# Kernel tuning notes

Hardware: AMD Instinct MI355X
Metric: run time of the kernel (lower is better)

The kernel has to match this reference:

```python
import jax, jax.numpy as jnp
import numpy as np

COUNT_CLIP_MAX = 1000.0

def _mlp2(x, w1, b1, w2, b2):
    # sg2im-style build_mlp with final_nonlinearity=True: relu after every linear
    h = jax.nn.relu(x @ w1 + b1)
    return jax.nn.relu(h @ w2 + b2)

def setup_inputs() -> dict:
    key = jax.random.key(0)
    ks = jax.random.split(key, 12)
    O, T, D, H = 100000, 400000, 128, 128
    D_out = D
    obj_vecs = jax.random.normal(ks[0], (O, D), dtype=jnp.float32)
    predi_vecs = jax.random.normal(ks[1], (T, D), dtype=jnp.float32)
    edges = jax.random.randint(ks[2], (T, 2), 0, O, dtype=jnp.int32)
    s = 0.02
    # net1: [3D, H, 2H + D_out]
    w1a = jax.random.normal(ks[3], (3 * D, H), dtype=jnp.float32) * s
    b1a = jnp.zeros((H,), dtype=jnp.float32)
    w1b = jax.random.normal(ks[4], (H, 2 * H + D_out), dtype=jnp.float32) * s
    b1b = jnp.zeros((2 * H + D_out,), dtype=jnp.float32)
    # net2: [H, H, D_out]
    w2a = jax.random.normal(ks[5], (H, H), dtype=jnp.float32) * s
    b2a = jnp.zeros((H,), dtype=jnp.float32)
    w2b = jax.random.normal(ks[6], (H, D_out), dtype=jnp.float32) * s
    b2b = jnp.zeros((D_out,), dtype=jnp.float32)
    return dict(obj_vecs=obj_vecs, predi_vecs=predi_vecs, edges=edges,
                w1a=w1a, b1a=b1a, w1b=w1b, b1b=b1b,
                w2a=w2a, b2a=b2a, w2b=w2b, b2b=b2b)

def reference(obj_vecs, predi_vecs, edges, w1a, b1a, w1b, b1b, w2a, b2a, w2b, b2b):
    O = obj_vecs.shape[0]
    H = w1a.shape[1]
    D_out = w2b.shape[1]
    s_idx = edges[:, 0]
    o_idx = edges[:, 1]
    # gather subject/object vectors, concat with predicate vecs: (T, 3D)
    cur_t_vecs = jnp.concatenate([obj_vecs[s_idx], predi_vecs, obj_vecs[o_idx]], axis=1)
    new_t_vecs = _mlp2(cur_t_vecs, w1a, b1a, w1b, b1b)  # (T, 2H + D_out)
    new_s_vecs = new_t_vecs[:, :H]
    new_p_vecs = new_t_vecs[:, H:H + D_out]
    new_o_vecs = new_t_vecs[:, H + D_out:2 * H + D_out]
    # scatter-add back to objects
    pooled = jnp.zeros((O, H), dtype=obj_vecs.dtype)
    pooled = pooled.at[s_idx].add(new_s_vecs).at[o_idx].add(new_o_vecs)
    # avg pooling: divide by clipped incidence counts
    ones = jnp.ones(s_idx.shape[0], dtype=obj_vecs.dtype)
    counts = jnp.zeros((O,), dtype=obj_vecs.dtype).at[s_idx].add(ones).at[o_idx].add(ones)
    counts = jnp.clip(counts, 1.0, COUNT_CLIP_MAX)
    pooled = pooled / counts[:, None]
    new_obj_vecs = _mlp2(pooled, w2a, b2a, w2b, b2b)  # (O, D_out)
    return new_obj_vecs, new_p_vecs
```

## Files before the change

### kernel.cpp

```cpp
#include <hip/hip_runtime.h>

typedef __attribute__((ext_vector_type(8))) short bf16x8;
typedef __attribute__((ext_vector_type(4))) float f32x4;
typedef __attribute__((ext_vector_type(4))) unsigned short u16x4;

#define MFMA __builtin_amdgcn_mfma_f32_16x16x32_bf16

__device__ __forceinline__ unsigned short f2bf(float x) {
    union { float f; unsigned u; } v; v.f = x;
    unsigned r = v.u + 0x7FFFu + ((v.u >> 16) & 1u);
    return (unsigned short)(r >> 16);
}
__device__ __forceinline__ float bf2f(unsigned short h) {
    union { unsigned u; float f; } v; v.u = ((unsigned)h) << 16;
    return v.f;
}

__global__ void pack_new(const float* __restrict__ w1a, const float* __restrict__ w1b,
                         const float* __restrict__ w2a, const float* __restrict__ w2b,
                         unsigned short* __restrict__ pk)
{
    const int b = blockIdx.x, l = threadIdx.x;
    unsigned short* ph;
    unsigned short* pl;
    int tile;
    bf16x8 hv, lv;

    if (b < 64) {
        tile = b;
        ph = pk; pl = pk + 64 * 512;
        int kc = tile >> 4, ct = tile & 15;
#pragma unroll
        for (int j = 0; j < 8; ++j) {
            int k = kc * 32 + (l >> 4) * 8 + j;
            int n = ct * 16 + (l & 15);
            float v = (n < 128) ? w1a[(size_t)k * 128 + n]
                                : w1a[(size_t)(256 + k) * 128 + (n - 128)];
            unsigned short h = f2bf(v);
            hv[j] = (short)h; lv[j] = (short)f2bf(v - bf2f(h));
        }
    } else if (b < 96) {
        tile = b - 64;
        ph = pk + 2 * 64 * 512; pl = ph + 32 * 512;
        int kc = tile >> 3, ct = tile & 7;
#pragma unroll
        for (int j = 0; j < 8; ++j) {
            int k = kc * 32 + (l >> 4) * 8 + j;
            int n = ct * 16 + (l & 15);
            float v = w1a[(size_t)(128 + k) * 128 + n];
            unsigned short h = f2bf(v);
            hv[j] = (short)h; lv[j] = (short)f2bf(v - bf2f(h));
        }
    } else if (b < 192) {
        tile = b - 96;
        ph = pk + 2 * 64 * 512 + 2 * 32 * 512; pl = ph + 96 * 512;
        int kc = tile / 24, ct = tile % 24;
#pragma unroll
        for (int j = 0; j < 8; ++j) {
            int k = kc * 32 + (l >> 4) * 8 + j;
            int n = ct * 16 + (l & 15);
            float v = w1b[(size_t)k * 384 + n];
            unsigned short h = f2bf(v);
            hv[j] = (short)h; lv[j] = (short)f2bf(v - bf2f(h));
        }
    } else if (b < 224) {
        tile = b - 192;
        ph = pk + 2 * 64 * 512 + 2 * 32 * 512 + 2 * 96 * 512; pl = ph + 32 * 512;
        int kc = tile >> 3, ct = tile & 7;
#pragma unroll
        for (int j = 0; j < 8; ++j) {
            int k = kc * 32 + (l >> 4) * 8 + j;
            int n = ct * 16 + (l & 15);
            float v = w2a[(size_t)k * 128 + n];
            unsigned short h = f2bf(v);
            hv[j] = (short)h; lv[j] = (short)f2bf(v - bf2f(h));
        }
    } else {
        tile = b - 224;
        ph = pk + 2 * 64 * 512 + 2 * 32 * 512 + 2 * 96 * 512 + 2 * 32 * 512; pl = ph + 32 * 512;
        int kc = tile >> 3, ct = tile & 7;
#pragma unroll
        for (int j = 0; j < 8; ++j) {
            int k = kc * 32 + (l >> 4) * 8 + j;
            int n = ct * 16 + (l & 15);
            float v = w2b[(size_t)k * 128 + n];
            unsigned short h = f2bf(v);
            hv[j] = (short)h; lv[j] = (short)f2bf(v - bf2f(h));
        }
    }
    *(bf16x8*)&ph[(size_t)(tile * 64 + l) * 8] = hv;
    *(bf16x8*)&pl[(size_t)(tile * 64 + l) * 8] = lv;
}

__global__ __launch_bounds__(512, 4) void obj_pre_kernel(
    const float* __restrict__ obj,
    const unsigned short* __restrict__ pkc_h, const unsigned short* __restrict__ pkc_l,
    float* __restrict__ A_tb, int O)
{
    __shared__ __align__(16) unsigned short Xh[64 * 128];
    __shared__ __align__(16) unsigned short Xl[64 * 128];

    const int tid = threadIdx.x;
    const int w = tid >> 6, l = tid & 63;
    const int rh = w & 1, cg = w >> 1;
    const int r0 = blockIdx.x * 64;

#pragma unroll
    for (int it = 0; it < 4; ++it) {
        int q = it * 512 + tid;
        int row = q >> 5, c4 = (q & 31) * 4;
        int rg = r0 + row; if (rg > O - 1) rg = O - 1;
        float4 v = *(const float4*)&obj[(size_t)rg * 128 + c4];
        u16x4 hv, lv; unsigned short h;
        h = f2bf(v.x); hv[0] = h; lv[0] = f2bf(v.x - bf2f(h));
        h = f2bf(v.y); hv[1] = h; lv[1] = f2bf(v.y - bf2f(h));
        h = f2bf(v.z); hv[2] = h; lv[2] = f2bf(v.z - bf2f(h));
        h = f2bf(v.w); hv[3] = h; lv[3] = f2bf(v.w - bf2f(h));
        int pc = row * 128 + (c4 ^ ((row & 7) << 3));
        *(u16x4*)&Xh[pc] = hv;
        *(u16x4*)&Xl[pc] = lv;
    }
    __syncthreads();

    f32x4 acc[2][4];
#pragma unroll
    for (int i = 0; i < 2; ++i)
#pragma unroll
        for (int j = 0; j < 4; ++j) acc[i][j] = (f32x4)0.0f;

#pragma unroll
    for (int kc = 0; kc < 4; ++kc) {
        bf16x8 ah[2], al[2];
#pragma unroll
        for (int rt = 0; rt < 2; ++rt) {
            int row = (rh * 2 + rt) * 16 + (l & 15);
            int col0 = kc * 32 + (l >> 4) * 8;
            int pc = row * 128 + (col0 ^ ((row & 7) << 3));
            ah[rt] = *(const bf16x8*)&Xh[pc];
            al[rt] = *(const bf16x8*)&Xl[pc];
        }
#pragma unroll
        for (int ct = 0; ct < 4; ++ct) {
            const int tile = kc * 16 + cg * 4 + ct;
            bf16x8 bh = *(const bf16x8*)&pkc_h[(size_t)(tile * 64 + l) * 8];
            bf16x8 bl = *(const bf16x8*)&pkc_l[(size_t)(tile * 64 + l) * 8];
#pragma unroll
            for (int rt = 0; rt < 2; ++rt) {
                acc[rt][ct] = MFMA(ah[rt], bh, acc[rt][ct], 0, 0, 0);
                acc[rt][ct] = MFMA(ah[rt], bl, acc[rt][ct], 0, 0, 0);
                acc[rt][ct] = MFMA(al[rt], bh, acc[rt][ct], 0, 0, 0);
            }
        }
    }

#pragma unroll
    for (int ct = 0; ct < 4; ++ct) {
        int col = cg * 64 + ct * 16 + (l & 15);
#pragma unroll
        for (int rt = 0; rt < 2; ++rt) {
#pragma unroll
            for (int r = 0; r < 4; ++r) {
                int row = (rh * 2 + rt) * 16 + (l >> 4) * 4 + r;
                if (r0 + row < O)
                    A_tb[(size_t)(r0 + row) * 256 + col] = acc[rt][ct][r];
            }
        }
    }
}

__global__ __launch_bounds__(512, 4) void triple_mlp_mfma2(
    const float* __restrict__ A_tb, const float* __restrict__ predi,
    const int* __restrict__ edges,
    const float* __restrict__ b1a, const float* __restrict__ b1b,
    const unsigned short* __restrict__ pkm_h, const unsigned short* __restrict__ pkm_l,
    const unsigned short* __restrict__ pk1b_h, const unsigned short* __restrict__ pk1b_l,
    float* __restrict__ pooled, float* __restrict__ out_p,
    float* __restrict__ counts, int T)
{
    __shared__ __align__(16) char SB[64 * 132 * 4];
    float (*G)[132] = (float (*)[132])SB;
    unsigned short* Xh = (unsigned short*)SB;
    unsigned short* Xl = (unsigned short*)(SB + 64 * 128 * 2);
    __shared__ int sIdx[64], oIdx[64];

    const int tid = threadIdx.x;
    const int w = tid >> 6, l = tid & 63;
    const int rh = w & 1, cg = w >> 1;
    const int t0 = blockIdx.x * 64;

    if (tid < 64) {
        int t = t0 + tid; int tc = (t < T) ? t : (T - 1);
        sIdx[tid] = edges[2 * tc];
        oIdx[tid] = edges[2 * tc + 1];
    }
    __syncthreads();

    if (tid < 64)        { if (t0 + tid      < T) atomicAdd(&counts[sIdx[tid]],      1.0f); }
    else if (tid < 128)  { if (t0 + tid - 64 < T) atomicAdd(&counts[oIdx[tid - 64]], 1.0f); }

#pragma unroll
    for (int it = 0; it < 4; ++it) {
        int q = it * 512 + tid;
        int row = q >> 5, c4 = (q & 31) * 4;
        float4 a = *(const float4*)&A_tb[(size_t)sIdx[row] * 256 + c4];
        float4 b = *(const float4*)&A_tb[(size_t)oIdx[row] * 256 + 128 + c4];
        float4 bb = *(const float4*)&b1a[c4];
        float4 g;
        g.x = a.x + b.x + bb.x; g.y = a.y + b.y + bb.y;
        g.z = a.z + b.z + bb.z; g.w = a.w + b.w + bb.w;
        *(float4*)&G[row][c4] = g;
    }
    __syncthreads();

    f32x4 acc1[2][2];
#pragma unroll
    for (int rt = 0; rt < 2; ++rt)
#pragma unroll
        for (int c2 = 0; c2 < 2; ++c2) {
            int col = cg * 32 + c2 * 16 + (l & 15);
#pragma unroll
            for (int r = 0; r < 4; ++r) {
                int row = (rh * 2 + rt) * 16 + (l >> 4) * 4 + r;
                acc1[rt][c2][r] = G[row][col];
            }
        }
    __syncthreads();

#pragma unroll
    for (int it = 0; it < 4; ++it) {
        int q = it * 512 + tid;
        int row = q >> 5, c4 = (q & 31) * 4;
        int t = t0 + row; int tc = (t < T) ? t : (T - 1);
        float4 v = *(const float4*)&predi[(size_t)tc * 128 + c4];
        u16x4 hv, lv; unsigned short h;
        h = f2bf(v.x); hv[0] = h; lv[0] = f2bf(v.x - bf2f(h));
        h = f2bf(v.y); hv[1] = h; lv[1] = f2bf(v.y - bf2f(h));
        h = f2bf(v.z); hv[2] = h; lv[2] = f2bf(v.z - bf2f(h));
        h = f2bf(v.w); hv[3] = h; lv[3] = f2bf(v.w - bf2f(h));
        int pc = row * 128 + (c4 ^ ((row & 7) << 3));
        *(u16x4*)&Xh[pc] = hv;
        *(u16x4*)&Xl[pc] = lv;
    }
    __syncthreads();

#pragma unroll
    for (int kc = 0; kc < 4; ++kc) {
        bf16x8 ah[2], al[2];
#pragma unroll
        for (int rt = 0; rt < 2; ++rt) {
            int row = (rh * 2 + rt) * 16 + (l & 15);
            int col0 = kc * 32 + (l >> 4) * 8;
            int pc = row * 128 + (col0 ^ ((row & 7) << 3));
            ah[rt] = *(const bf16x8*)&Xh[pc];
            al[rt] = *(const bf16x8*)&Xl[pc];
        }
#pragma unroll
        for (int c2 = 0; c2 < 2; ++c2) {
            const int tile = kc * 8 + cg * 2 + c2;
            bf16x8 bh = *(const bf16x8*)&pkm_h[(size_t)(tile * 64 + l) * 8];
            bf16x8 bl = *(const bf16x8*)&pkm_l[(size_t)(tile * 64 + l) * 8];
#pragma unroll
            for (int rt = 0; rt < 2; ++rt) {
                acc1[rt][c2] = MFMA(ah[rt], bh, acc1[rt][c2], 0, 0, 0);
                acc1[rt][c2] = MFMA(ah[rt], bl, acc1[rt][c2], 0, 0, 0);
                acc1[rt][c2] = MFMA(al[rt], bh, acc1[rt][c2], 0, 0, 0);
            }
        }
    }
    __syncthreads();

#pragma unroll
    for (int c2 = 0; c2 < 2; ++c2) {
        int col = cg * 32 + c2 * 16 + (l & 15);
#pragma unroll
        for (int rt = 0; rt < 2; ++rt) {
#pragma unroll
            for (int r = 0; r < 4; ++r) {
                int row = (rh * 2 + rt) * 16 + (l >> 4) * 4 + r;
                float h = fmaxf(acc1[rt][c2][r], 0.0f);
                unsigned short hh = f2bf(h);
                unsigned short hl = f2bf(h - bf2f(hh));
                int pc = row * 128 + (col ^ ((row & 7) << 3));
                Xh[pc] = hh; Xl[pc] = hl;
            }
        }
    }
    __syncthreads();

    f32x4 acc2[2][6];
#pragma unroll
    for (int i = 0; i < 2; ++i)
#pragma unroll
        for (int j = 0; j < 6; ++j) acc2[i][j] = (f32x4)0.0f;

#pragma unroll
    for (int kc = 0; kc < 4; ++kc) {
        bf16x8 ah[2], al[2];
#pragma unroll
        for (int rt = 0; rt < 2; ++rt) {
            int row = (rh * 2 + rt) * 16 + (l & 15);
            int col0 = kc * 32 + (l >> 4) * 8;
            int pc = row * 128 + (col0 ^ ((row & 7) << 3));
            ah[rt] = *(const bf16x8*)&Xh[pc];
            al[rt] = *(const bf16x8*)&Xl[pc];
        }
#pragma unroll
        for (int ct = 0; ct < 6; ++ct) {
            const int tile = kc * 24 + cg * 6 + ct;
            bf16x8 bh = *(const bf16x8*)&pk1b_h[(size_t)(tile * 64 + l) * 8];
            bf16x8 bl = *(const bf16x8*)&pk1b_l[(size_t)(tile * 64 + l) * 8];
#pragma unroll
            for (int rt = 0; rt < 2; ++rt) {
                acc2[rt][ct] = MFMA(ah[rt], bh, acc2[rt][ct], 0, 0, 0);
                acc2[rt][ct] = MFMA(ah[rt], bl, acc2[rt][ct], 0, 0, 0);
                acc2[rt][ct] = MFMA(al[rt], bh, acc2[rt][ct], 0, 0, 0);
            }
        }
    }

#pragma unroll
    for (int ct = 0; ct < 6; ++ct) {
        int col = cg * 96 + ct * 16 + (l & 15);
        float bb = b1b[col];
#pragma unroll
        for (int rt = 0; rt < 2; ++rt) {
#pragma unroll
            for (int r = 0; r < 4; ++r) {
                int row = (rh * 2 + rt) * 16 + (l >> 4) * 4 + r;
                if (t0 + row >= T) continue;
                float v = fmaxf(acc2[rt][ct][r] + bb, 0.0f);
                if (col < 128)
                    atomicAdd(&pooled[(size_t)sIdx[row] * 128 + col], v);
                else if (col < 256)
                    out_p[(size_t)(t0 + row) * 128 + (col - 128)] = v;
                else
                    atomicAdd(&pooled[(size_t)oIdx[row] * 128 + (col - 256)], v);
            }
        }
    }
}

__global__ __launch_bounds__(512, 4) void obj_mlp_mfma(
    const float* __restrict__ b2a, const float* __restrict__ b2b,
    const unsigned short* __restrict__ pk2a_h, const unsigned short* __restrict__ pk2a_l,
    const unsigned short* __restrict__ pk2b_h, const unsigned short* __restrict__ pk2b_l,
    float* __restrict__ io, const float* __restrict__ counts, int O)
{
    __shared__ __align__(16) unsigned short Xh[64 * 128];
    __shared__ __align__(16) unsigned short Xl[64 * 128];

    const int tid = threadIdx.x;
    const int w = tid >> 6, l = tid & 63;
    const int rh = w & 1, cg = w >> 1;
    const int r0 = blockIdx.x * 64;

#pragma unroll
    for (int it = 0; it < 4; ++it) {
        int q = it * 512 + tid;
        int row = q >> 5, c4 = (q & 31) * 4;
        int rg = r0 + row; if (rg > O - 1) rg = O - 1;
        float c = counts[rg];
        c = fminf(fmaxf(c, 1.0f), 1000.0f);
        float inv = 1.0f / c;
        float4 v = *(const float4*)&io[(size_t)rg * 128 + c4];
        v.x *= inv; v.y *= inv; v.z *= inv; v.w *= inv;
        u16x4 hv, lv; unsigned short h;
        h = f2bf(v.x); hv[0] = h; lv[0] = f2bf(v.x - bf2f(h));
        h = f2bf(v.y); hv[1] = h; lv[1] = f2bf(v.y - bf2f(h));
        h = f2bf(v.z); hv[2] = h; lv[2] = f2bf(v.z - bf2f(h));
        h = f2bf(v.w); hv[3] = h; lv[3] = f2bf(v.w - bf2f(h));
        int pc = row * 128 + (c4 ^ ((row & 7) << 3));
        *(u16x4*)&Xh[pc] = hv;
        *(u16x4*)&Xl[pc] = lv;
    }
    __syncthreads();

    f32x4 acc[2][2];
#pragma unroll
    for (int i = 0; i < 2; ++i) { acc[i][0] = (f32x4)0.0f; acc[i][1] = (f32x4)0.0f; }

#pragma unroll
    for (int kc = 0; kc < 4; ++kc) {
        bf16x8 ah[2], al[2];
#pragma unroll
        for (int rt = 0; rt < 2; ++rt) {
            int row = (rh * 2 + rt) * 16 + (l & 15);
            int col0 = kc * 32 + (l >> 4) * 8;
            int pc = row * 128 + (col0 ^ ((row & 7) << 3));
            ah[rt] = *(const bf16x8*)&Xh[pc];
            al[rt] = *(const bf16x8*)&Xl[pc];
        }
#pragma unroll
        for (int c2 = 0; c2 < 2; ++c2) {
            const int tile = kc * 8 + cg * 2 + c2;
            bf16x8 bh = *(const bf16x8*)&pk2a_h[(size_t)(tile * 64 + l) * 8];
            bf16x8 bl = *(const bf16x8*)&pk2a_l[(size_t)(tile * 64 + l) * 8];
#pragma unroll
            for (int rt = 0; rt < 2; ++rt) {
                acc[rt][c2] = MFMA(ah[rt], bh, acc[rt][c2], 0, 0, 0);
                acc[rt][c2] = MFMA(ah[rt], bl, acc[rt][c2], 0, 0, 0);
                acc[rt][c2] = MFMA(al[rt], bh, acc[rt][c2], 0, 0, 0);
            }
        }
    }
    __syncthreads();

#pragma unroll
    for (int c2 = 0; c2 < 2; ++c2) {
        int col = cg * 32 + c2 * 16 + (l & 15);
        float bb = b2a[col];
#pragma unroll
        for (int rt = 0; rt < 2; ++rt) {
#pragma unroll
            for (int r = 0; r < 4; ++r) {
                int row = (rh * 2 + rt) * 16 + (l >> 4) * 4 + r;
                float h = fmaxf(acc[rt][c2][r] + bb, 0.0f);
                unsigned short hh = f2bf(h);
                unsigned short hl = f2bf(h - bf2f(hh));
                int pc = row * 128 + (col ^ ((row & 7) << 3));
                Xh[pc] = hh; Xl[pc] = hl;
            }
        }
    }
    __syncthreads();

    f32x4 acc2[2][2];
#pragma unroll
    for (int i = 0; i < 2; ++i) { acc2[i][0] = (f32x4)0.0f; acc2[i][1] = (f32x4)0.0f; }

#pragma unroll
    for (int kc = 0; kc < 4; ++kc) {
        bf16x8 ah[2], al[2];
#pragma unroll
        for (int rt = 0; rt < 2; ++rt) {
            int row = (rh * 2 + rt) * 16 + (l & 15);
            int col0 = kc * 32 + (l >> 4) * 8;
            int pc = row * 128 + (col0 ^ ((row & 7) << 3));
            ah[rt] = *(const bf16x8*)&Xh[pc];
            al[rt] = *(const bf16x8*)&Xl[pc];
        }
#pragma unroll
        for (int c2 = 0; c2 < 2; ++c2) {
            const int tile = kc * 8 + cg * 2 + c2;
            bf16x8 bh = *(const bf16x8*)&pk2b_h[(size_t)(tile * 64 + l) * 8];
            bf16x8 bl = *(const bf16x8*)&pk2b_l[(size_t)(tile * 64 + l) * 8];
#pragma unroll
            for (int rt = 0; rt < 2; ++rt) {
                acc2[rt][c2] = MFMA(ah[rt], bh, acc2[rt][c2], 0, 0, 0);
                acc2[rt][c2] = MFMA(ah[rt], bl, acc2[rt][c2], 0, 0, 0);
                acc2[rt][c2] = MFMA(al[rt], bh, acc2[rt][c2], 0, 0, 0);
            }
        }
    }

#pragma unroll
    for (int c2 = 0; c2 < 2; ++c2) {
        int col = cg * 32 + c2 * 16 + (l & 15);
        float bb = b2b[col];
#pragma unroll
        for (int rt = 0; rt < 2; ++rt) {
#pragma unroll
            for (int r = 0; r < 4; ++r) {
                int row = (rh * 2 + rt) * 16 + (l >> 4) * 4 + r;
                if (r0 + row >= O) continue;
                float v = fmaxf(acc2[rt][c2][r] + bb, 0.0f);
                io[(size_t)(r0 + row) * 128 + col] = v;
            }
        }
    }
}

__global__ void pack_weights(const float* __restrict__ w1a, const float* __restrict__ w1b,
                             const float* __restrict__ w2a, const float* __restrict__ w2b,
                             unsigned short* __restrict__ pk)
{
    const int b = blockIdx.x, l = threadIdx.x;
    const float* W; int N, tile; unsigned short *ph, *pl;
    if (b < 96)       { W = w1a; N = 128; tile = b;       ph = pk;                 pl = pk + 96*512; }
    else if (b < 192) { W = w1b; N = 384; tile = b - 96;  ph = pk + 2*96*512;      pl = pk + 3*96*512; }
    else if (b < 224) { W = w2a; N = 128; tile = b - 192; ph = pk + 4*96*512;      pl = pk + 4*96*512 + 32*512; }
    else              { W = w2b; N = 128; tile = b - 224; ph = pk + 4*96*512 + 2*32*512; pl = pk + 4*96*512 + 3*32*512; }
    const int tpr = N / 16;
    const int kc = tile / tpr, ct = tile % tpr;
    bf16x8 hv, lv;
#pragma unroll
    for (int j = 0; j < 8; ++j) {
        int k = kc * 32 + (l >> 4) * 8 + j;
        int n = ct * 16 + (l & 15);
        float v = W[(size_t)k * N + n];
        unsigned short h = f2bf(v);
        hv[j] = (short)h;
        lv[j] = (short)f2bf(v - bf2f(h));
    }
    *(bf16x8*)&ph[(size_t)(tile * 64 + l) * 8] = hv;
    *(bf16x8*)&pl[(size_t)(tile * 64 + l) * 8] = lv;
}

__global__ __launch_bounds__(512, 4) void triple_mlp_mfma(
    const float* __restrict__ obj, const float* __restrict__ predi,
    const int* __restrict__ edges,
    const float* __restrict__ b1a, const float* __restrict__ b1b,
    const unsigned short* __restrict__ pk1a_h, const unsigned short* __restrict__ pk1a_l,
    const unsigned short* __restrict__ pk1b_h, const unsigned short* __restrict__ pk1b_l,
    float* __restrict__ pooled, float* __restrict__ out_p,
    float* __restrict__ counts, int T)
{
    __shared__ __align__(16) unsigned short Xh[64 * 128];
    __shared__ __align__(16) unsigned short Xl[64 * 128];
    __shared__ int sIdx[64], oIdx[64];

    const int tid = threadIdx.x;
    const int w = tid >> 6, l = tid & 63;
    const int rh = w & 1, cg = w >> 1;
    const int t0 = blockIdx.x * 64;

    if (tid < 64) {
        int t = t0 + tid; int tc = (t < T) ? t : (T - 1);
        sIdx[tid] = edges[2 * tc];
        oIdx[tid] = edges[2 * tc + 1];
    }
    __syncthreads();

    if (tid < 64)        { if (t0 + tid      < T) atomicAdd(&counts[sIdx[tid]],      1.0f); }
    else if (tid < 128)  { if (t0 + tid - 64 < T) atomicAdd(&counts[oIdx[tid - 64]], 1.0f); }

    f32x4 acc1[2][2];
#pragma unroll
    for (int i = 0; i < 2; ++i) { acc1[i][0] = (f32x4)0.0f; acc1[i][1] = (f32x4)0.0f; }

#pragma unroll
    for (int s = 0; s < 3; ++s) {
#pragma unroll
        for (int it = 0; it < 4; ++it) {
            int q = it * 512 + tid;
            int row = q >> 5, c4 = (q & 31) * 4;
            int t = t0 + row; int tc = (t < T) ? t : (T - 1);
            const float* src = (s == 0) ? obj   + (size_t)sIdx[row] * 128 + c4
                             : (s == 1) ? predi + (size_t)tc        * 128 + c4
                                        : obj   + (size_t)oIdx[row] * 128 + c4;
            float4 v = *(const float4*)src;
            u16x4 hv, lv; unsigned short h;
            h = f2bf(v.x); hv[0] = h; lv[0] = f2bf(v.x - bf2f(h));
            h = f2bf(v.y); hv[1] = h; lv[1] = f2bf(v.y - bf2f(h));
            h = f2bf(v.z); hv[2] = h; lv[2] = f2bf(v.z - bf2f(h));
            h = f2bf(v.w); hv[3] = h; lv[3] = f2bf(v.w - bf2f(h));
            int pc = row * 128 + (c4 ^ ((row & 7) << 3));
            *(u16x4*)&Xh[pc] = hv;
            *(u16x4*)&Xl[pc] = lv;
        }
        __syncthreads();

#pragma unroll
        for (int kc2 = 0; kc2 < 4; ++kc2) {
            const int kcg = s * 4 + kc2;
            bf16x8 ah[2], al[2];
#pragma unroll
            for (int rt = 0; rt < 2; ++rt) {
                int row = (rh * 2 + rt) * 16 + (l & 15);
                int col0 = kc2 * 32 + (l >> 4) * 8;
                int pc = row * 128 + (col0 ^ ((row & 7) << 3));
                ah[rt] = *(const bf16x8*)&Xh[pc];
                al[rt] = *(const bf16x8*)&Xl[pc];
            }
#pragma unroll
            for (int c2 = 0; c2 < 2; ++c2) {
                const int tile = kcg * 8 + cg * 2 + c2;
                bf16x8 bh = *(const bf16x8*)&pk1a_h[(size_t)(tile * 64 + l) * 8];
                bf16x8 bl = *(const bf16x8*)&pk1a_l[(size_t)(tile * 64 + l) * 8];
#pragma unroll
                for (int rt = 0; rt < 2; ++rt) {
                    acc1[rt][c2] = MFMA(ah[rt], bh, acc1[rt][c2], 0, 0, 0);
                    acc1[rt][c2] = MFMA(ah[rt], bl, acc1[rt][c2], 0, 0, 0);
                    acc1[rt][c2] = MFMA(al[rt], bh, acc1[rt][c2], 0, 0, 0);
                }
            }
        }
        __syncthreads();
    }

#pragma unroll
    for (int c2 = 0; c2 < 2; ++c2) {
        int col = cg * 32 + c2 * 16 + (l & 15);
        float bb = b1a[col];
#pragma unroll
        for (int rt = 0; rt < 2; ++rt) {
#pragma unroll
            for (int r = 0; r < 4; ++r) {
                int row = (rh * 2 + rt) * 16 + (l >> 4) * 4 + r;
                float h = fmaxf(acc1[rt][c2][r] + bb, 0.0f);
                unsigned short hh = f2bf(h);
                unsigned short hl = f2bf(h - bf2f(hh));
                int pc = row * 128 + (col ^ ((row & 7) << 3));
                Xh[pc] = hh; Xl[pc] = hl;
            }
        }
    }
    __syncthreads();

    f32x4 acc2[2][6];
#pragma unroll
    for (int i = 0; i < 2; ++i)
#pragma unroll
        for (int j = 0; j < 6; ++j) acc2[i][j] = (f32x4)0.0f;

#pragma unroll
    for (int kc = 0; kc < 4; ++kc) {
        bf16x8 ah[2], al[2];
#pragma unroll
        for (int rt = 0; rt < 2; ++rt) {
            int row = (rh * 2 + rt) * 16 + (l & 15);
            int col0 = kc * 32 + (l >> 4) * 8;
            int pc = row * 128 + (col0 ^ ((row & 7) << 3));
            ah[rt] = *(const bf16x8*)&Xh[pc];
            al[rt] = *(const bf16x8*)&Xl[pc];
        }
#pragma unroll
        for (int ct = 0; ct < 6; ++ct) {
            const int tile = kc * 24 + cg * 6 + ct;
            bf16x8 bh = *(const bf16x8*)&pk1b_h[(size_t)(tile * 64 + l) * 8];
            bf16x8 bl = *(const bf16x8*)&pk1b_l[(size_t)(tile * 64 + l) * 8];
#pragma unroll
            for (int rt = 0; rt < 2; ++rt) {
                acc2[rt][ct] = MFMA(ah[rt], bh, acc2[rt][ct], 0, 0, 0);
                acc2[rt][ct] = MFMA(ah[rt], bl, acc2[rt][ct], 0, 0, 0);
                acc2[rt][ct] = MFMA(al[rt], bh, acc2[rt][ct], 0, 0, 0);
            }
        }
    }

#pragma unroll
    for (int ct = 0; ct < 6; ++ct) {
        int col = cg * 96 + ct * 16 + (l & 15);
        float bb = b1b[col];
#pragma unroll
        for (int rt = 0; rt < 2; ++rt) {
#pragma unroll
            for (int r = 0; r < 4; ++r) {
                int row = (rh * 2 + rt) * 16 + (l >> 4) * 4 + r;
                if (t0 + row >= T) continue;
                float v = fmaxf(acc2[rt][ct][r] + bb, 0.0f);
                if (col < 128)
                    atomicAdd(&pooled[(size_t)sIdx[row] * 128 + col], v);
                else if (col < 256)
                    out_p[(size_t)(t0 + row) * 128 + (col - 128)] = v;
                else
                    atomicAdd(&pooled[(size_t)oIdx[row] * 128 + (col - 256)], v);
            }
        }
    }
}

extern "C" void kernel_launch(void* const* d_in, const int* in_sizes, int n_in,
                              void* d_out, int out_size, void* d_ws, size_t ws_size,
                              hipStream_t stream) {
    const float* obj   = (const float*)d_in[0];
    const float* predi = (const float*)d_in[1];
    const int*   edges = (const int*)d_in[2];
    const float* w1a   = (const float*)d_in[3];
    const float* b1a   = (const float*)d_in[4];
    const float* w1b   = (const float*)d_in[5];
    const float* b1b   = (const float*)d_in[6];
    const float* w2a   = (const float*)d_in[7];
    const float* b2a   = (const float*)d_in[8];
    const float* w2b   = (const float*)d_in[9];
    const float* b2b   = (const float*)d_in[10];
    (void)n_in; (void)out_size;

    const int O = in_sizes[0] / 128;
    const int T = in_sizes[1] / 128;

    float* out    = (float*)d_out;
    float* pooled = out;
    float* out_p  = out + (size_t)O * 128;
    float* counts = (float*)d_ws;
    unsigned short* pk = (unsigned short*)(counts + O);

    hipMemsetAsync(pooled, 0, (size_t)O * 128 * sizeof(float), stream);
    hipMemsetAsync(counts, 0, (size_t)O * sizeof(float), stream);

    const size_t need = (size_t)O * 4 + (size_t)512 * 512 * 2 + (size_t)O * 256 * 4;

    if (ws_size >= need) {
        unsigned short* pkc_h  = pk;
        unsigned short* pkc_l  = pkc_h  + 64 * 512;
        unsigned short* pkm_h  = pkc_l  + 64 * 512;
        unsigned short* pkm_l  = pkm_h  + 32 * 512;
        unsigned short* pk1b_h = pkm_l  + 32 * 512;
        unsigned short* pk1b_l = pk1b_h + 96 * 512;
        unsigned short* pk2a_h = pk1b_l + 96 * 512;
        unsigned short* pk2a_l = pk2a_h + 32 * 512;
        unsigned short* pk2b_h = pk2a_l + 32 * 512;
        unsigned short* pk2b_l = pk2b_h + 32 * 512;
        float* A_tb = (float*)(pk + (size_t)512 * 512);

        pack_new<<<256, 64, 0, stream>>>(w1a, w1b, w2a, w2b, pk);
        obj_pre_kernel<<<(O + 63) / 64, 512, 0, stream>>>(obj, pkc_h, pkc_l, A_tb, O);
        triple_mlp_mfma2<<<(T + 63) / 64, 512, 0, stream>>>(
            A_tb, predi, edges, b1a, b1b,
            pkm_h, pkm_l, pk1b_h, pk1b_l,
            pooled, out_p, counts, T);
        obj_mlp_mfma<<<(O + 63) / 64, 512, 0, stream>>>(
            b2a, b2b, pk2a_h, pk2a_l, pk2b_h, pk2b_l, pooled, counts, O);
    } else {
        unsigned short* pk1a_h = pk;
        unsigned short* pk1a_l = pk1a_h + 96 * 512;
        unsigned short* pk1b_h = pk1a_l + 96 * 512;
        unsigned short* pk1b_l = pk1b_h + 96 * 512;
        unsigned short* pk2a_h = pk1b_l + 96 * 512;
        unsigned short* pk2a_l = pk2a_h + 32 * 512;
        unsigned short* pk2b_h = pk2a_l + 32 * 512;
        unsigned short* pk2b_l = pk2b_h + 32 * 512;

        pack_weights<<<256, 64, 0, stream>>>(w1a, w1b, w2a, w2b, pk);
        triple_mlp_mfma<<<(T + 63) / 64, 512, 0, stream>>>(
            obj, predi, edges, b1a, b1b,
            pk1a_h, pk1a_l, pk1b_h, pk1b_l,
            pooled, out_p, counts, T);
        obj_mlp_mfma<<<(O + 63) / 64, 512, 0, stream>>>(
            b2a, b2b, pk2a_h, pk2a_l, pk2b_h, pk2b_l, pooled, counts, O);
    }
}
```

Measured before the change: 1.028 ms.

## Store precomputed projections and pooled accumulator in bf16 with packed bf16 atomics

Changes the intermediate per-object projection buffer A_tb from fp32 to bf16, which halves the gather traffic in the triple kernel. It also switches the scatter-add pooling buffer to bf16 and uses global_atomic_pk_add_bf16 on lane-paired values exchanged through shuffles, so each atomic covers two columns. Pooled output now goes to a separate workspace buffer rather than the output, the fallback path is removed, and launch bounds are raised to 8 waves per SIMD. The cost is lower accumulation precision: bf16 atomic sums over many edges can drift from the fp32 reference.

New measurement: 1.429 ms. 38.9% more time.

```diff
diff --git a/kernel.cpp b/kernel.cpp
--- a/kernel.cpp
+++ b/kernel.cpp
@@ -14,6 +14,9 @@
 __device__ __forceinline__ float bf2f(unsigned short h) {
     union { unsigned u; float f; } v; v.u = ((unsigned)h) << 16;
     return v.f;
+}
+__device__ __forceinline__ void atom_pk_bf16(unsigned short* p, unsigned v2) {
+    asm volatile("global_atomic_pk_add_bf16 %0, %1, off sc1" :: "v"(p), "v"(v2) : "memory");
 }
 
 __global__ void pack_new(const float* __restrict__ w1a, const float* __restrict__ w1b,
@@ -95,7 +98,7 @@
 __global__ __launch_bounds__(512, 4) void obj_pre_kernel(
     const float* __restrict__ obj,
     const unsigned short* __restrict__ pkc_h, const unsigned short* __restrict__ pkc_l,
-    float* __restrict__ A_tb, int O)
+    unsigned short* __restrict__ A_tb, int O)
 {
     __shared__ __align__(16) unsigned short Xh[64 * 128];
     __shared__ __align__(16) unsigned short Xl[64 * 128];
@@ -156,25 +159,36 @@
 #pragma unroll
     for (int ct = 0; ct < 4; ++ct) {
         int col = cg * 64 + ct * 16 + (l & 15);
-#pragma unroll
-        for (int rt = 0; rt < 2; ++rt) {
-#pragma unroll
-            for (int r = 0; r < 4; ++r) {
-                int row = (rh * 2 + rt) * 16 + (l >> 4) * 4 + r;
+        int cb = col & ~1;
+#pragma unroll
+        for (int rt = 0; rt < 2; ++rt) {
+            float v[4], p[4];
+#pragma unroll
+            for (int r = 0; r < 4; ++r) v[r] = acc[rt][ct][r];
+#pragma unroll
+            for (int r = 0; r < 4; ++r) p[r] = __shfl_xor(v[r], 1, 64);
+            int base = (rh * 2 + rt) * 16 + (l >> 4) * 4;
+#pragma unroll
+            for (int k = 0; k < 2; ++k) {
+                int rr = (l & 1) * 2 + k;
+                int row = base + rr;
+                float lo = (l & 1) ? p[rr] : v[rr];
+                float hi = (l & 1) ? v[rr] : p[rr];
+                unsigned u = (unsigned)f2bf(lo) | ((unsigned)f2bf(hi) << 16);
                 if (r0 + row < O)
-                    A_tb[(size_t)(r0 + row) * 256 + col] = acc[rt][ct][r];
-            }
-        }
-    }
-}
-
-__global__ __launch_bounds__(512, 4) void triple_mlp_mfma2(
-    const float* __restrict__ A_tb, const float* __restrict__ predi,
+                    *(unsigned*)&A_tb[(size_t)(r0 + row) * 256 + cb] = u;
+            }
+        }
+    }
+}
+
+__global__ __launch_bounds__(512, 8) void triple_mlp_mfma2(
+    const unsigned short* __restrict__ A_tb, const float* __restrict__ predi,
     const int* __restrict__ edges,
     const float* __restrict__ b1a, const float* __restrict__ b1b,
     const unsigned short* __restrict__ pkm_h, const unsigned short* __restrict__ pkm_l,
     const unsigned short* __restrict__ pk1b_h, const unsigned short* __restrict__ pk1b_l,
-    float* __restrict__ pooled, float* __restrict__ out_p,
+    unsigned short* __restrict__ pooled, float* __restrict__ out_p,
     float* __restrict__ counts, int T)
 {
     __shared__ __align__(16) char SB[64 * 132 * 4];
@@ -199,16 +213,20 @@
     else if (tid < 128)  { if (t0 + tid - 64 < T) atomicAdd(&counts[oIdx[tid - 64]], 1.0f); }
 
 #pragma unroll
-    for (int it = 0; it < 4; ++it) {
+    for (int it = 0; it < 2; ++it) {
         int q = it * 512 + tid;
-        int row = q >> 5, c4 = (q & 31) * 4;
-        float4 a = *(const float4*)&A_tb[(size_t)sIdx[row] * 256 + c4];
-        float4 b = *(const float4*)&A_tb[(size_t)oIdx[row] * 256 + 128 + c4];
-        float4 bb = *(const float4*)&b1a[c4];
-        float4 g;
-        g.x = a.x + b.x + bb.x; g.y = a.y + b.y + bb.y;
-        g.z = a.z + b.z + bb.z; g.w = a.w + b.w + bb.w;
-        *(float4*)&G[row][c4] = g;
+        int row = q >> 4, c8 = (q & 15) * 8;
+        bf16x8 a = *(const bf16x8*)&A_tb[(size_t)sIdx[row] * 256 + c8];
+        bf16x8 b = *(const bf16x8*)&A_tb[(size_t)oIdx[row] * 256 + 128 + c8];
+        float bb[8];
+        *(float4*)&bb[0] = *(const float4*)&b1a[c8];
+        *(float4*)&bb[4] = *(const float4*)&b1a[c8 + 4];
+        float g[8];
+#pragma unroll
+        for (int j = 0; j < 8; ++j)
+            g[j] = bf2f((unsigned short)a[j]) + bf2f((unsigned short)b[j]) + bb[j];
+        *(float4*)&G[row][c8]     = *(float4*)&g[0];
+        *(float4*)&G[row][c8 + 4] = *(float4*)&g[4];
     }
     __syncthreads();
 
@@ -324,27 +342,44 @@
         float bb = b1b[col];
 #pragma unroll
         for (int rt = 0; rt < 2; ++rt) {
-#pragma unroll
-            for (int r = 0; r < 4; ++r) {
-                int row = (rh * 2 + rt) * 16 + (l >> 4) * 4 + r;
-                if (t0 + row >= T) continue;
-                float v = fmaxf(acc2[rt][ct][r] + bb, 0.0f);
-                if (col < 128)
-                    atomicAdd(&pooled[(size_t)sIdx[row] * 128 + col], v);
-                else if (col < 256)
-                    out_p[(size_t)(t0 + row) * 128 + (col - 128)] = v;
-                else
-                    atomicAdd(&pooled[(size_t)oIdx[row] * 128 + (col - 256)], v);
-            }
-        }
-    }
-}
-
-__global__ __launch_bounds__(512, 4) void obj_mlp_mfma(
+            float v[4];
+#pragma unroll
+            for (int r = 0; r < 4; ++r) v[r] = fmaxf(acc2[rt][ct][r] + bb, 0.0f);
+            int base = (rh * 2 + rt) * 16 + (l >> 4) * 4;
+            if (col >= 128 && col < 256) {
+#pragma unroll
+                for (int r = 0; r < 4; ++r) {
+                    int row = base + r;
+                    if (t0 + row < T)
+                        out_p[(size_t)(t0 + row) * 128 + (col - 128)] = v[r];
+                }
+            } else {
+                float p[4];
+#pragma unroll
+                for (int r = 0; r < 4; ++r) p[r] = __shfl_xor(v[r], 1, 64);
+                const int* IDX = (col < 128) ? sIdx : oIdx;
+                int cb = ((col < 128) ? col : col - 256) & ~1;
+#pragma unroll
+                for (int k = 0; k < 2; ++k) {
+                    int rr = (l & 1) * 2 + k;
+                    int row = base + rr;
+                    float lo = (l & 1) ? p[rr] : v[rr];
+                    float hi = (l & 1) ? v[rr] : p[rr];
+                    unsigned u = (unsigned)f2bf(lo) | ((unsigned)f2bf(hi) << 16);
+                    if (t0 + row < T)
+                        atom_pk_bf16(pooled + (size_t)IDX[row] * 128 + cb, u);
+                }
+            }
+        }
+    }
+}
+
+__global__ __launch_bounds__(512, 8) void obj_mlp_mfma(
     const float* __restrict__ b2a, const float* __restrict__ b2b,
     const unsigned short* __restrict__ pk2a_h, const unsigned short* __restrict__ pk2a_l,
     const unsigned short* __restrict__ pk2b_h, const unsigned short* __restrict__ pk2b_l,
-    float* __restrict__ io, const float* __restrict__ counts, int O)
+    const unsigned short* __restrict__ pooled, const float* __restrict__ counts,
+    float* __restrict__ out, int O)
 {
     __shared__ __align__(16) unsigned short Xh[64 * 128];
     __shared__ __align__(16) unsigned short Xl[64 * 128];
@@ -355,23 +390,25 @@
     const int r0 = blockIdx.x * 64;
 
 #pragma unroll
-    for (int it = 0; it < 4; ++it) {
+    for (int it = 0; it < 2; ++it) {
         int q = it * 512 + tid;
-        int row = q >> 5, c4 = (q & 31) * 4;
+        int row = q >> 4, c8 = (q & 15) * 8;
         int rg = r0 + row; if (rg > O - 1) rg = O - 1;
         float c = counts[rg];
         c = fminf(fmaxf(c, 1.0f), 1000.0f);
         float inv = 1.0f / c;
-        float4 v = *(const float4*)&io[(size_t)rg * 128 + c4];
-        v.x *= inv; v.y *= inv; v.z *= inv; v.w *= inv;
-        u16x4 hv, lv; unsigned short h;
-        h = f2bf(v.x); hv[0] = h; lv[0] = f2bf(v.x - bf2f(h));
-        h = f2bf(v.y); hv[1] = h; lv[1] = f2bf(v.y - bf2f(h));
-        h = f2bf(v.z); hv[2] = h; lv[2] = f2bf(v.z - bf2f(h));
-        h = f2bf(v.w); hv[3] = h; lv[3] = f2bf(v.w - bf2f(h));
-        int pc = row * 128 + (c4 ^ ((row & 7) << 3));
-        *(u16x4*)&Xh[pc] = hv;
-        *(u16x4*)&Xl[pc] = lv;
+        bf16x8 pv = *(const bf16x8*)&pooled[(size_t)rg * 128 + c8];
+        bf16x8 hv, lv;
+#pragma unroll
+        for (int j = 0; j < 8; ++j) {
+            float f = bf2f((unsigned short)pv[j]) * inv;
+            unsigned short hh = f2bf(f);
+            hv[j] = (short)hh;
+            lv[j] = (short)f2bf(f - bf2f(hh));
+        }
+        int pc = row * 128 + (c8 ^ ((row & 7) << 3));
+        *(bf16x8*)&Xh[pc] = hv;
+        *(bf16x8*)&Xl[pc] = lv;
     }
     __syncthreads();
 
@@ -464,187 +501,7 @@
                 int row = (rh * 2 + rt) * 16 + (l >> 4) * 4 + r;
                 if (r0 + row >= O) continue;
                 float v = fmaxf(acc2[rt][c2][r] + bb, 0.0f);
-                io[(size_t)(r0 + row) * 128 + col] = v;
-            }
-        }
-    }
-}
-
-__global__ void pack_weights(const float* __restrict__ w1a, const float* __restrict__ w1b,
-                             const float* __restrict__ w2a, const float* __restrict__ w2b,
-                             unsigned short* __restrict__ pk)
-{
-    const int b = blockIdx.x, l = threadIdx.x;
-    const float* W; int N, tile; unsigned short *ph, *pl;
-    if (b < 96)       { W = w1a; N = 128; tile = b;       ph = pk;                 pl = pk + 96*512; }
-    else if (b < 192) { W = w1b; N = 384; tile = b - 96;  ph = pk + 2*96*512;      pl = pk + 3*96*512; }
-    else if (b < 224) { W = w2a; N = 128; tile = b - 192; ph = pk + 4*96*512;      pl = pk + 4*96*512 + 32*512; }
-    else              { W = w2b; N = 128; tile = b - 224; ph = pk + 4*96*512 + 2*32*512; pl = pk + 4*96*512 + 3*32*512; }
-    const int tpr = N / 16;
-    const int kc = tile / tpr, ct = tile % tpr;
-    bf16x8 hv, lv;
-#pragma unroll
-    for (int j = 0; j < 8; ++j) {
-        int k = kc * 32 + (l >> 4) * 8 + j;
-        int n = ct * 16 + (l & 15);
-        float v = W[(size_t)k * N + n];
-        unsigned short h = f2bf(v);
-        hv[j] = (short)h;
-        lv[j] = (short)f2bf(v - bf2f(h));
-    }
-    *(bf16x8*)&ph[(size_t)(tile * 64 + l) * 8] = hv;
-    *(bf16x8*)&pl[(size_t)(tile * 64 + l) * 8] = lv;
-}
-
-__global__ __launch_bounds__(512, 4) void triple_mlp_mfma(
-    const float* __restrict__ obj, const float* __restrict__ predi,
-    const int* __restrict__ edges,
-    const float* __restrict__ b1a, const float* __restrict__ b1b,
-    const unsigned short* __restrict__ pk1a_h, const unsigned short* __restrict__ pk1a_l,
-    const unsigned short* __restrict__ pk1b_h, const unsigned short* __restrict__ pk1b_l,
-    float* __restrict__ pooled, float* __restrict__ out_p,
-    float* __restrict__ counts, int T)
-{
-    __shared__ __align__(16) unsigned short Xh[64 * 128];
-    __shared__ __align__(16) unsigned short Xl[64 * 128];
-    __shared__ int sIdx[64], oIdx[64];
-
-    const int tid = threadIdx.x;
-    const int w = tid >> 6, l = tid & 63;
-    const int rh = w & 1, cg = w >> 1;
-    const int t0 = blockIdx.x * 64;
-
-    if (tid < 64) {
-        int t = t0 + tid; int tc = (t < T) ? t : (T - 1);
-        sIdx[tid] = edges[2 * tc];
-        oIdx[tid] = edges[2 * tc + 1];
-    }
-    __syncthreads();
-
-    if (tid < 64)        { if (t0 + tid      < T) atomicAdd(&counts[sIdx[tid]],      1.0f); }
-    else if (tid < 128)  { if (t0 + tid - 64 < T) atomicAdd(&counts[oIdx[tid - 64]], 1.0f); }
-
-    f32x4 acc1[2][2];
-#pragma unroll
-    for (int i = 0; i < 2; ++i) { acc1[i][0] = (f32x4)0.0f; acc1[i][1] = (f32x4)0.0f; }
-
-#pragma unroll
-    for (int s = 0; s < 3; ++s) {
-#pragma unroll
-        for (int it = 0; it < 4; ++it) {
-            int q = it * 512 + tid;
-            int row = q >> 5, c4 = (q & 31) * 4;
-            int t = t0 + row; int tc = (t < T) ? t : (T - 1);
-            const float* src = (s == 0) ? obj   + (size_t)sIdx[row] * 128 + c4
-                             : (s == 1) ? predi + (size_t)tc        * 128 + c4
-                                        : obj   + (size_t)oIdx[row] * 128 + c4;
-            float4 v = *(const float4*)src;
-            u16x4 hv, lv; unsigned short h;
-            h = f2bf(v.x); hv[0] = h; lv[0] = f2bf(v.x - bf2f(h));
-            h = f2bf(v.y); hv[1] = h; lv[1] = f2bf(v.y - bf2f(h));
-            h = f2bf(v.z); hv[2] = h; lv[2] = f2bf(v.z - bf2f(h));
-            h = f2bf(v.w); hv[3] = h; lv[3] = f2bf(v.w - bf2f(h));
-            int pc = row * 128 + (c4 ^ ((row & 7) << 3));
-            *(u16x4*)&Xh[pc] = hv;
-            *(u16x4*)&Xl[pc] = lv;
-        }
-        __syncthreads();
-
-#pragma unroll
-        for (int kc2 = 0; kc2 < 4; ++kc2) {
-            const int kcg = s * 4 + kc2;
-            bf16x8 ah[2], al[2];
-#pragma unroll
-            for (int rt = 0; rt < 2; ++rt) {
-                int row = (rh * 2 + rt) * 16 + (l & 15);
-                int col0 = kc2 * 32 + (l >> 4) * 8;
-                int pc = row * 128 + (col0 ^ ((row & 7) << 3));
-                ah[rt] = *(const bf16x8*)&Xh[pc];
-                al[rt] = *(const bf16x8*)&Xl[pc];
-            }
-#pragma unroll
-            for (int c2 = 0; c2 < 2; ++c2) {
-                const int tile = kcg * 8 + cg * 2 + c2;
-                bf16x8 bh = *(const bf16x8*)&pk1a_h[(size_t)(tile * 64 + l) * 8];
-                bf16x8 bl = *(const bf16x8*)&pk1a_l[(size_t)(tile * 64 + l) * 8];
-#pragma unroll
-                for (int rt = 0; rt < 2; ++rt) {
-                    acc1[rt][c2] = MFMA(ah[rt], bh, acc1[rt][c2], 0, 0, 0);
-                    acc1[rt][c2] = MFMA(ah[rt], bl, acc1[rt][c2], 0, 0, 0);
-                    acc1[rt][c2] = MFMA(al[rt], bh, acc1[rt][c2], 0, 0, 0);
-                }
-            }
-        }
-        __syncthreads();
-    }
-
-#pragma unroll
-    for (int c2 = 0; c2 < 2; ++c2) {
-        int col = cg * 32 + c2 * 16 + (l & 15);
-        float bb = b1a[col];
-#pragma unroll
-        for (int rt = 0; rt < 2; ++rt) {
-#pragma unroll
-            for (int r = 0; r < 4; ++r) {
-                int row = (rh * 2 + rt) * 16 + (l >> 4) * 4 + r;
-                float h = fmaxf(acc1[rt][c2][r] + bb, 0.0f);
-                unsigned short hh = f2bf(h);
-                unsigned short hl = f2bf(h - bf2f(hh));
-                int pc = row * 128 + (col ^ ((row & 7) << 3));
-                Xh[pc] = hh; Xl[pc] = hl;
-            }
-        }
-    }
-    __syncthreads();
-
-    f32x4 acc2[2][6];
-#pragma unroll
-    for (int i = 0; i < 2; ++i)
-#pragma unroll
-        for (int j = 0; j < 6; ++j) acc2[i][j] = (f32x4)0.0f;
-
-#pragma unroll
-    for (int kc = 0; kc < 4; ++kc) {
-        bf16x8 ah[2], al[2];
-#pragma unroll
-        for (int rt = 0; rt < 2; ++rt) {
-            int row = (rh * 2 + rt) * 16 + (l & 15);
-            int col0 = kc * 32 + (l >> 4) * 8;
-            int pc = row * 128 + (col0 ^ ((row & 7) << 3));
-            ah[rt] = *(const bf16x8*)&Xh[pc];
-            al[rt] = *(const bf16x8*)&Xl[pc];
-        }
-#pragma unroll
-        for (int ct = 0; ct < 6; ++ct) {
-            const int tile = kc * 24 + cg * 6 + ct;
-            bf16x8 bh = *(const bf16x8*)&pk1b_h[(size_t)(tile * 64 + l) * 8];
-            bf16x8 bl = *(const bf16x8*)&pk1b_l[(size_t)(tile * 64 + l) * 8];
-#pragma unroll
-            for (int rt = 0; rt < 2; ++rt) {
-                acc2[rt][ct] = MFMA(ah[rt], bh, acc2[rt][ct], 0, 0, 0);
-                acc2[rt][ct] = MFMA(ah[rt], bl, acc2[rt][ct], 0, 0, 0);
-                acc2[rt][ct] = MFMA(al[rt], bh, acc2[rt][ct], 0, 0, 0);
-            }
-        }
-    }
-
-#pragma unroll
-    for (int ct = 0; ct < 6; ++ct) {
-        int col = cg * 96 + ct * 16 + (l & 15);
-        float bb = b1b[col];
-#pragma unroll
-        for (int rt = 0; rt < 2; ++rt) {
-#pragma unroll
-            for (int r = 0; r < 4; ++r) {
-                int row = (rh * 2 + rt) * 16 + (l >> 4) * 4 + r;
-                if (t0 + row >= T) continue;
-                float v = fmaxf(acc2[rt][ct][r] + bb, 0.0f);
-                if (col < 128)
-                    atomicAdd(&pooled[(size_t)sIdx[row] * 128 + col], v);
-                else if (col < 256)
-                    out_p[(size_t)(t0 + row) * 128 + (col - 128)] = v;
-                else
-                    atomicAdd(&pooled[(size_t)oIdx[row] * 128 + (col - 256)], v);
+                out[(size_t)(r0 + row) * 128 + col] = v;
             }
         }
     }
@@ -664,59 +521,40 @@
     const float* b2a   = (const float*)d_in[8];
     const float* w2b   = (const float*)d_in[9];
     const float* b2b   = (const float*)d_in[10];
-    (void)n_in; (void)out_size;
+    (void)n_in; (void)out_size; (void)ws_size;
 
     const int O = in_sizes[0] / 128;
     const int T = in_sizes[1] / 128;
 
-    float* out    = (float*)d_out;
-    float* pooled = out;
-    float* out_p  = out + (size_t)O * 128;
+    float* out     = (float*)d_out;
+    float* new_obj = out;
+    float* out_p   = out + (size_t)O * 128;
+
     float* counts = (float*)d_ws;
-    unsigned short* pk = (unsigned short*)(counts + O);
-
-    hipMemsetAsync(pooled, 0, (size_t)O * 128 * sizeof(float), stream);
+    unsigned short* pk     = (unsigned short*)(counts + O);
+    unsigned short* pooled = pk + (size_t)512 * 512;
+    unsigned short* A_tb   = pooled + (size_t)O * 128;
+
+    unsigned short* pkc_h  = pk;
+    unsigned short* pkc_l  = pkc_h  + 64 * 512;
+    unsigned short* pkm_h  = pkc_l  + 64 * 512;
+    unsigned short* pkm_l  = pkm_h  + 32 * 512;
+    unsigned short* pk1b_h = pkm_l  + 32 * 512;
+    unsigned short* pk1b_l = pk1b_h + 96 * 512;
+    unsigned short* pk2a_h = pk1b_l + 96 * 512;
+    unsigned short* pk2a_l = pk2a_h + 32 * 512;
+    unsigned short* pk2b_h = pk2a_l + 32 * 512;
+    unsigned short* pk2b_l = pk2b_h + 32 * 512;
+
     hipMemsetAsync(counts, 0, (size_t)O * sizeof(float), stream);
-
-    const size_t need = (size_t)O * 4 + (size_t)512 * 512 * 2 + (size_t)O * 256 * 4;
-
-    if (ws_size >= need) {
-        unsigned short* pkc_h  = pk;
-        unsigned short* pkc_l  = pkc_h  + 64 * 512;
-        unsigned short* pkm_h  = pkc_l  + 64 * 512;
-        unsigned short* pkm_l  = pkm_h  + 32 * 512;
-        unsigned short* pk1b_h = pkm_l  + 32 * 512;
-        unsigned short* pk1b_l = pk1b_h + 96 * 512;
-        unsigned short* pk2a_h = pk1b_l + 96 * 512;
-        unsigned short* pk2a_l = pk2a_h + 32 * 512;
-        unsigned short* pk2b_h = pk2a_l + 32 * 512;
-        unsigned short* pk2b_l = pk2b_h + 32 * 512;
-        float* A_tb = (float*)(pk + (size_t)512 * 512);
-
-        pack_new<<<256, 64, 0, stream>>>(w1a, w1b, w2a, w2b, pk);
-        obj_pre_kernel<<<(O + 63) / 64, 512, 0, stream>>>(obj, pkc_h, pkc_l, A_tb, O);
-        triple_mlp_mfma2<<<(T + 63) / 64, 512, 0, stream>>>(
-            A_tb, predi, edges, b1a, b1b,
-            pkm_h, pkm_l, pk1b_h, pk1b_l,
-            pooled, out_p, counts, T);
-        obj_mlp_mfma<<<(O + 63) / 64, 512, 0, stream>>>(
-            b2a, b2b, pk2a_h, pk2a_l, pk2b_h, pk2b_l, pooled, counts, O);
-    } else {
-        unsigned short* pk1a_h = pk;
-        unsigned short* pk1a_l = pk1a_h + 96 * 512;
-        unsigned short* pk1b_h = pk1a_l + 96 * 512;
-        unsigned short* pk1b_l = pk1b_h + 96 * 512;
-        unsigned short* pk2a_h = pk1b_l + 96 * 512;
-        unsigned short* pk2a_l = pk2a_h + 32 * 512;
-        unsigned short* pk2b_h = pk2a_l + 32 * 512;
-        unsigned short* pk2b_l = pk2b_h + 32 * 512;
-
-        pack_weights<<<256, 64, 0, stream>>>(w1a, w1b, w2a, w2b, pk);
-        triple_mlp_mfma<<<(T + 63) / 64, 512, 0, stream>>>(
-            obj, predi, edges, b1a, b1b,
-            pk1a_h, pk1a_l, pk1b_h, pk1b_l,
-            pooled, out_p, counts, T);
-        obj_mlp_mfma<<<(O + 63) / 64, 512, 0, stream>>>(
-            b2a, b2b, pk2a_h, pk2a_l, pk2b_h, pk2b_l, pooled, counts, O);
-    }
-}
+    hipMemsetAsync(pooled, 0, (size_t)O * 128 * sizeof(unsigned short), stream);
+
+    pack_new<<<256, 64, 0, stream>>>(w1a, w1b, w2a, w2b, pk);
+    obj_pre_kernel<<<(O + 63) / 64, 512, 0, stream>>>(obj, pkc_h, pkc_l, A_tb, O);
+    triple_mlp_mfma2<<<(T + 63) / 64, 512, 0, stream>>>(
+        A_tb, predi, edges, b1a, b1b,
+        pkm_h, pkm_l, pk1b_h, pk1b_l,
+        pooled, out_p, counts, T);
+    obj_mlp_mfma<<<(O + 63) / 64, 512, 0, stream>>>(
+        b2a, b2b, pk2a_h, pk2a_l, pk2b_h, pk2b_l, pooled, counts, new_obj, O);
+}
```
